# Kernel optimization log

Measured on AMD Instinct MI355X. Metric: run time of the kernel, lower is better.

Reference implementation:

```python
import jax, jax.numpy as jnp
import numpy as np

B, T, DM, DF, E, K = 4, 1024, 768, 3072, 8, 2


def setup_inputs() -> dict:
    key = jax.random.key(0)
    k0, k1, k2, k3 = jax.random.split(key, 4)
    x = jax.random.normal(k0, (B, T, DM), jnp.float32)
    Wg = jax.random.normal(k1, (DM, E), jnp.float32) * 0.02
    W1 = jax.random.normal(k2, (E, DM, DF), jnp.float32) * 0.02
    b1 = jnp.zeros((E, DF), jnp.float32)
    W2 = jax.random.normal(k3, (E, DF, DM), jnp.float32) * 0.02
    b2 = jnp.zeros((E, DM), jnp.float32)
    return {"x": x, "Wg": Wg, "W1": W1, "b1": b1, "W2": W2, "b2": b2}


def reference(x, Wg, W1, b1, W2, b2):
    # --- flatten (s)equence x (t)oken -> S tokens of width m ---
    m = x.shape[-1]
    xs = x.reshape(-1, m)              # [S, m]
    S = xs.shape[0]
    n_exp = W1.shape[0]

    # --- top-k softmax gate: combine_weights [k,S], dispatch order sorted by expert ---
    logits = xs @ Wg                   # [S, E]
    probs = jax.nn.softmax(logits, axis=-1)
    topv, topi = jax.lax.top_k(probs, K)                 # [S, K]
    cw = topv / jnp.sum(topv, axis=-1, keepdims=True)    # renormalize top-k
    combine_weights = cw.T                               # [K, S]

    # slot layout: slot = j*S + s (matches rerouted_output.reshape(k, S, m))
    eid_flat = topi.T.reshape(-1)                        # [S*K] expert id per slot
    dispatch_mask = jnp.argsort(eid_flat)                # stable sort by expert == chunked order
    e_sorted = eid_flat[dispatch_mask]                   # [S*K] sorted expert ids

    # --- dispatch: gather token rows (dispatch_mask % S indexes the token) ---
    dispatched = xs[dispatch_mask % S]                   # [S*K, m]

    # --- experts: per-expert FFN; loop over fixed small expert count, masked combine ---
    expert_outputs = jnp.zeros_like(dispatched)
    for e in range(n_exp):
        sel = (e_sorted == e)[:, None].astype(dispatched.dtype)
        h = jax.nn.relu(dispatched @ W1[e] + b1[e])      # [S*K, DF]
        expert_outputs = expert_outputs + sel * (h @ W2[e] + b2[e])

    # --- scatter back to slot order, then weighted combine over k ---
    rerouted = jnp.zeros((S * K, m), expert_outputs.dtype).at[dispatch_mask].set(expert_outputs)
    rerouted = rerouted.reshape(K, S, m)
    combined = jnp.einsum('ks,ksm->sm', combine_weights, rerouted)
    return combined.reshape(x.shape).astype(x.dtype)
```

## Files before the change

### kernel.cpp

```cpp
#include <hip/hip_runtime.h>
#include <math.h>

typedef short short8 __attribute__((ext_vector_type(8)));
typedef float f32x4 __attribute__((ext_vector_type(4)));
typedef unsigned short u16;
typedef unsigned int u32;

#define S_TOK 4096
#define DM 768
#define DF 3072
#define NE 8
#define NSLOT (S_TOK*2)
#define PSLOT 9216
#define MBMAX 72

#define WS_COUNTS   0
#define WS_CURSOR   512
#define WS_OFFS     1024
#define WS_MBE      1088
#define WS_EID      2048
#define WS_GW       (WS_EID + NSLOT*4)
#define WS_POS      (WS_GW  + NSLOT*4)
#define WS_TOK      (WS_POS + NSLOT*4)
#define CTRL_BYTES  262144

#define AS1 __attribute__((address_space(1)))
#define AS3 __attribute__((address_space(3)))
#define GLDS16(g, s) __builtin_amdgcn_global_load_lds((const AS1 u32*)(g), (AS3 u32*)(s), 16, 0, 0)

__device__ inline u16 f2b(float f){
    u32 u = __builtin_bit_cast(u32, f);
    u32 r = (u + 0x7fffu + ((u >> 16) & 1u)) >> 16;
    return (u16)r;
}

__global__ __launch_bounds__(256) void cvtw_kernel(const float* __restrict__ W1, u16* __restrict__ W1s,
                                                   const float* __restrict__ W2, u16* __restrict__ W2s,
                                                   int* __restrict__ counts, int* __restrict__ cursor){
    if (blockIdx.x == 0 && blockIdx.y == 0 && threadIdx.x < 128){
        counts[threadIdx.x] = 0; cursor[threadIdx.x] = 0;
    }
    int e = blockIdx.y;
    int b = blockIdx.x;
    const float* Wp; u16* Wsp; int Kd, Nd;
    if (b < 576){ Wp = W1; Wsp = W1s; Kd = DM; Nd = DF; }
    else        { b -= 576; Wp = W2; Wsp = W2s; Kd = DF; Nd = DM; }
    int kbn = Kd >> 5;
    Wp  += (size_t)e*Kd*Nd;
    Wsp += (size_t)e*Kd*Nd;
    int t = threadIdx.x;
    int u = b*256 + t;
    int l   = u & 63;
    int kb  = (u >> 6) % kbn;
    int qq  = (u >> 6) / kbn;
    int ntp = qq & 3;
    int nb  = qq >> 2;
    int k0 = kb*32 + (l >> 4)*8;
    int c  = nb*128 + ntp*32 + (l & 15);
    const float* src = Wp + (size_t)k0*Nd + c;
    short8 o0, o1;
#pragma unroll
    for (int j = 0; j < 8; j++){
        o0[j] = (short)f2b(src[(size_t)j*Nd]);
        o1[j] = (short)f2b(src[(size_t)j*Nd + 16]);
    }
    size_t v0 = ((size_t)(nb*8 + ntp*2)*kbn + kb)*64 + l;
    *(short8*)&Wsp[v0*8] = o0;
    *(short8*)&Wsp[v0*8 + (size_t)kbn*512] = o1;
}

#define GATE_BLOCKS 128
__global__ __launch_bounds__(256) void gate_kernel(const float* __restrict__ x, const float* __restrict__ Wg,
                                                   int* __restrict__ eid, float* __restrict__ gw,
                                                   int* __restrict__ counts, u16* __restrict__ xb){
    __shared__ int lh[NE];
    int t = threadIdx.x;
    if (t < NE) lh[t] = 0;
    __syncthreads();
    int wv = t >> 6, l = t & 63;
    int wgid = blockIdx.x*4 + wv;
    const int NW = GATE_BLOCKS*4;

    for (int s = wgid; s < S_TOK; s += NW){
        float acc[NE];
#pragma unroll
        for (int e = 0; e < NE; e++) acc[e] = 0.f;
        const float* xr = x + (size_t)s * DM;
        u16* xbr = xb + (size_t)s * DM;
#pragma unroll
        for (int i = 0; i < DM/64; i++){
            int d = l + 64*i;
            float xv = xr[d];
            xbr[d] = f2b(xv);
            float4 w0 = *(const float4*)(Wg + d*NE);
            float4 w1 = *(const float4*)(Wg + d*NE + 4);
            acc[0] += xv*w0.x; acc[1] += xv*w0.y; acc[2] += xv*w0.z; acc[3] += xv*w0.w;
            acc[4] += xv*w1.x; acc[5] += xv*w1.y; acc[6] += xv*w1.z; acc[7] += xv*w1.w;
        }
#pragma unroll
        for (int e = 0; e < NE; e++){
#pragma unroll
            for (int off = 32; off; off >>= 1) acc[e] += __shfl_down(acc[e], off);
        }
        if (l == 0){
            int i1 = 0; float v1 = acc[0];
            for (int e = 1; e < NE; e++) if (acc[e] > v1){ v1 = acc[e]; i1 = e; }
            int i2 = -1; float v2 = -1e30f;
            for (int e = 0; e < NE; e++) if (e != i1 && acc[e] > v2){ v2 = acc[e]; i2 = e; }
            float w0, w1;
            if (i2 < 0){ i2 = (i1 + 1) & 7; w0 = 1.f; w1 = 0.f; }
            else {
                float e2 = expf(v2 - v1);
                w0 = 1.f / (1.f + e2);
                w1 = e2 / (1.f + e2);
            }
            eid[2*s]   = i1; gw[2*s]   = w0;
            eid[2*s+1] = i2; gw[2*s+1] = w1;
            atomicAdd(&lh[i1], 1);
            atomicAdd(&lh[i2], 1);
        }
    }
    __syncthreads();
    if (t < NE && lh[t] > 0) atomicAdd(&counts[t*16], lh[t]);
}

__global__ void offsets_kernel(const int* __restrict__ counts, int* __restrict__ offs,
                               int* __restrict__ cursor, int* __restrict__ mbe){
    if (threadIdx.x == 0 && blockIdx.x == 0){
        int P = 0;
        for (int e = 0; e < NE; e++){
            offs[e] = P; cursor[e*16] = P;
            int padded = ((counts[e*16] + 127) >> 7) << 7;
            for (int mb = P >> 7; mb < (P + padded) >> 7; mb++) mbe[mb] = e;
            P += padded;
        }
        offs[NE] = P;
        for (int mb = P >> 7; mb < MBMAX; mb++) mbe[mb] = -1;
    }
}

__global__ __launch_bounds__(256) void scatter_kernel(const int* __restrict__ eid, int* __restrict__ cursor,
                                                      const int* __restrict__ counts, const int* __restrict__ offs,
                                                      const int* __restrict__ mbe,
                                                      int* __restrict__ tok_of, int* __restrict__ pos_of){
    __shared__ int lh[NE];
    __shared__ int base[NE];
    int t = threadIdx.x;
    if (t < NE) lh[t] = 0;
    __syncthreads();
    int i = blockIdx.x*256 + t;
    int e = 0, r = 0;
    if (i < NSLOT){
        e = eid[i];
        if (e < 0) e = 0; if (e > 7) e = 7;
        r = atomicAdd(&lh[e], 1);
    }
    __syncthreads();
    if (t < NE) base[t] = (lh[t] > 0) ? atomicAdd(&cursor[t*16], lh[t]) : 0;
    __syncthreads();
    if (i < NSLOT){
        int p = base[e] + r;
        if (p < 0) p = 0; if (p >= PSLOT) p = PSLOT - 1;
        tok_of[p] = i >> 1;
        pos_of[i] = p;
    }
    int p = i;
    int pe = mbe[p >> 7];
    if (pe < 0){ tok_of[p] = 0; }
    else if (p >= offs[pe] + counts[pe*16]){ tok_of[p] = 0; }
}

__global__ __launch_bounds__(256) void gemm1p_kernel(const u16* __restrict__ xb, const int* __restrict__ tok_of,
                                                     const int* __restrict__ mbe, const u16* __restrict__ W1s,
                                                     const float* __restrict__ b1, u16* __restrict__ h){
    const int KB = DM/32;
    const int NT = DM/64;
    int bid = blockIdx.x;
    int by = bid % 24, mb = bid / 24;
    int e = mbe[mb];
    if (e < 0) return;
    int m0 = mb*128, n0 = by*128;

    int t = threadIdx.x;
    int w = t >> 6, l = t & 63;
    int wm = w & 1, wn = w >> 1;

    __shared__ u16 As[128*72];
    __shared__ u16 Bs[2*2*8*512];

    int row0 = t >> 2, kc = t & 3;
    const u16* a0 = xb + (size_t)tok_of[m0 + row0]*DM + kc*8;
    const u16* a1 = xb + (size_t)tok_of[m0 + row0 + 64]*DM + kc*8;
    u16* as0 = &As[row0*72 + kc*8];
    u16* as1 = &As[(row0 + 64)*72 + kc*8];

    const u16* bbase = W1s + (size_t)e*DM*DF + (size_t)(((n0 >> 4) + 2*w)*KB)*512 + l*8;

#define STB1(kb2, buf) do{ \
    GLDS16(bbase + (size_t)(2*(kb2))*512,                   &Bs[(buf)*8192 + (2*w)*512]); \
    GLDS16(bbase + (size_t)(2*(kb2)+1)*512,                 &Bs[(buf)*8192 + 4096 + (2*w)*512]); \
    GLDS16(bbase + (size_t)KB*512 + (size_t)(2*(kb2))*512,  &Bs[(buf)*8192 + (2*w+1)*512]); \
    GLDS16(bbase + (size_t)KB*512 + (size_t)(2*(kb2)+1)*512,&Bs[(buf)*8192 + 4096 + (2*w+1)*512]); \
}while(0)

    f32x4 acc[4][4];
#pragma unroll
    for (int i = 0; i < 4; i++)
#pragma unroll
        for (int j = 0; j < 4; j++) acc[i][j] = (f32x4){0.f,0.f,0.f,0.f};

    short8 av0a = *(const short8*)a0;
    short8 av0b = *(const short8*)(a0 + 32);
    short8 av1a = *(const short8*)a1;
    short8 av1b = *(const short8*)(a1 + 32);
    STB1(0, 0);
    *(short8*)as0 = av0a; *(short8*)(as0 + 32) = av0b;
    *(short8*)as1 = av1a; *(short8*)(as1 + 32) = av1b;
    av0a = *(const short8*)(a0 + 64);
    av0b = *(const short8*)(a0 + 96);
    av1a = *(const short8*)(a1 + 64);
    av1b = *(const short8*)(a1 + 96);
    __builtin_amdgcn_sched_barrier(0);
    asm volatile("s_waitcnt vmcnt(4) lgkmcnt(0)" ::: "memory");
    __builtin_amdgcn_sched_barrier(0);
    __builtin_amdgcn_s_barrier();

    int cb = 0;
    for (int kt = 0; kt < NT; kt++){
        if (kt + 1 < NT) STB1(kt + 1, cb ^ 1);
#pragma unroll
        for (int ks = 0; ks < 2; ks++){
            short8 af[4], bf[4];
#pragma unroll
            for (int mt = 0; mt < 4; mt++)
                af[mt] = *(const short8*)&As[(wm*64 + mt*16 + (l & 15))*72 + ks*32 + (l >> 4)*8];
#pragma unroll
            for (int nt = 0; nt < 4; nt++)
                bf[nt] = *(const short8*)&Bs[cb*8192 + ks*4096 + (wn*4 + nt)*512 + l*8];
#pragma unroll
            for (int mt = 0; mt < 4; mt++)
#pragma unroll
                for (int nt = 0; nt < 4; nt++)
                    acc[mt][nt] = __builtin_amdgcn_mfma_f32_16x16x32_bf16(af[mt], bf[nt], acc[mt][nt], 0, 0, 0);
        }
        __builtin_amdgcn_sched_barrier(0);
        asm volatile("s_waitcnt vmcnt(4) lgkmcnt(0)" ::: "memory");
        __builtin_amdgcn_sched_barrier(0);
        __builtin_amdgcn_s_barrier();
        if (kt + 1 < NT){
            *(short8*)as0 = av0a; *(short8*)(as0 + 32) = av0b;
            *(short8*)as1 = av1a; *(short8*)(as1 + 32) = av1b;
            if (kt + 2 < NT){
                av0a = *(const short8*)(a0 + (kt+2)*64);
                av0b = *(const short8*)(a0 + (kt+2)*64 + 32);
                av1a = *(const short8*)(a1 + (kt+2)*64);
                av1b = *(const short8*)(a1 + (kt+2)*64 + 32);
                __builtin_amdgcn_sched_barrier(0);
                asm volatile("s_waitcnt vmcnt(4) lgkmcnt(0)" ::: "memory");
                __builtin_amdgcn_sched_barrier(0);
            } else {
                __builtin_amdgcn_sched_barrier(0);
                asm volatile("s_waitcnt vmcnt(0) lgkmcnt(0)" ::: "memory");
                __builtin_amdgcn_sched_barrier(0);
            }
            __builtin_amdgcn_s_barrier();
        }
        cb ^= 1;
    }
#undef STB1

#pragma unroll
    for (int nt = 0; nt < 4; nt++){
        int col = n0 + wn*64 + nt*16 + (l & 15);
        float bv = b1[e*DF + col];
#pragma unroll
        for (int mt = 0; mt < 4; mt++){
#pragma unroll
            for (int r = 0; r < 4; r++){
                int grow = m0 + wm*64 + mt*16 + (l >> 4)*4 + r;
                float v = acc[mt][nt][r] + bv;
                v = v > 0.f ? v : 0.f;
                h[(size_t)grow*DF + col] = f2b(v);
            }
        }
    }
}

__global__ __launch_bounds__(256) void gemm2p_kernel(const u16* __restrict__ h, const int* __restrict__ mbe,
                                                     const u16* __restrict__ W2s, const float* __restrict__ b2,
                                                     float* __restrict__ y){
    const int KB = DF/32;
    const int NT = DF/64;
    int bid = blockIdx.x;
    int mb = bid % MBMAX;
    int by = bid / MBMAX;
    int e = mbe[mb];
    if (e < 0) return;
    int m0 = mb*128, n0 = by*128;

    int t = threadIdx.x;
    int w = t >> 6, l = t & 63;
    int wm = w & 1, wn = w >> 1;

    __shared__ u16 As[128*72];
    __shared__ u16 Bs[3*2*8*512];

    int row0 = t >> 2, kc = t & 3;
    const u16* a0 = h + (size_t)(m0 + row0)*DF + kc*8;
    const u16* a1 = h + (size_t)(m0 + row0 + 64)*DF + kc*8;
    u16* as0 = &As[row0*72 + kc*8];
    u16* as1 = &As[(row0 + 64)*72 + kc*8];

    const u16* bbase = W2s + (size_t)e*DF*DM + (size_t)(((n0 >> 4) + 2*w)*KB)*512 + l*8;

#define STB2(kb2, buf) do{ \
    GLDS16(bbase + (size_t)(2*(kb2))*512,                   &Bs[(buf)*8192 + (2*w)*512]); \
    GLDS16(bbase + (size_t)(2*(kb2)+1)*512,                 &Bs[(buf)*8192 + 4096 + (2*w)*512]); \
    GLDS16(bbase + (size_t)KB*512 + (size_t)(2*(kb2))*512,  &Bs[(buf)*8192 + (2*w+1)*512]); \
    GLDS16(bbase + (size_t)KB*512 + (size_t)(2*(kb2)+1)*512,&Bs[(buf)*8192 + 4096 + (2*w+1)*512]); \
}while(0)

    f32x4 acc[4][4];
#pragma unroll
    for (int i = 0; i < 4; i++)
#pragma unroll
        for (int j = 0; j < 4; j++) acc[i][j] = (f32x4){0.f,0.f,0.f,0.f};

    short8 av0a = *(const short8*)a0;
    short8 av0b = *(const short8*)(a0 + 32);
    short8 av1a = *(const short8*)a1;
    short8 av1b = *(const short8*)(a1 + 32);
    STB2(0, 0);
    STB2(1, 1);
    *(short8*)as0 = av0a; *(short8*)(as0 + 32) = av0b;
    *(short8*)as1 = av1a; *(short8*)(as1 + 32) = av1b;
    av0a = *(const short8*)(a0 + 64);
    av0b = *(const short8*)(a0 + 96);
    av1a = *(const short8*)(a1 + 64);
    av1b = *(const short8*)(a1 + 96);
    __builtin_amdgcn_sched_barrier(0);
    asm volatile("s_waitcnt vmcnt(8) lgkmcnt(0)" ::: "memory");
    __builtin_amdgcn_sched_barrier(0);
    __builtin_amdgcn_s_barrier();

    int cb = 0, sb = 2;
    for (int kt = 0; kt < NT; kt++){
        if (kt + 2 < NT) STB2(kt + 2, sb);
#pragma unroll
        for (int ks = 0; ks < 2; ks++){
            short8 af[4], bf[4];
#pragma unroll
            for (int mt = 0; mt < 4; mt++)
                af[mt] = *(const short8*)&As[(wm*64 + mt*16 + (l & 15))*72 + ks*32 + (l >> 4)*8];
#pragma unroll
            for (int nt = 0; nt < 4; nt++)
                bf[nt] = *(const short8*)&Bs[cb*8192 + ks*4096 + (wn*4 + nt)*512 + l*8];
#pragma unroll
            for (int mt = 0; mt < 4; mt++)
#pragma unroll
                for (int nt = 0; nt < 4; nt++)
                    acc[mt][nt] = __builtin_amdgcn_mfma_f32_16x16x32_bf16(af[mt], bf[nt], acc[mt][nt], 0, 0, 0);
        }
        __builtin_amdgcn_sched_barrier(0);
        asm volatile("s_waitcnt vmcnt(4) lgkmcnt(0)" ::: "memory");
        __builtin_amdgcn_sched_barrier(0);
        __builtin_amdgcn_s_barrier();
        if (kt + 1 < NT){
            *(short8*)as0 = av0a; *(short8*)(as0 + 32) = av0b;
            *(short8*)as1 = av1a; *(short8*)(as1 + 32) = av1b;
            if (kt + 2 < NT){
                av0a = *(const short8*)(a0 + (kt+2)*64);
                av0b = *(const short8*)(a0 + (kt+2)*64 + 32);
                av1a = *(const short8*)(a1 + (kt+2)*64);
                av1b = *(const short8*)(a1 + (kt+2)*64 + 32);
            }
            __builtin_amdgcn_sched_barrier(0);
            asm volatile("s_waitcnt lgkmcnt(0)" ::: "memory");
            __builtin_amdgcn_sched_barrier(0);
            __builtin_amdgcn_s_barrier();
        }
        cb = (cb == 2) ? 0 : cb + 1;
        sb = (sb == 2) ? 0 : sb + 1;
    }
#undef STB2

#pragma unroll
    for (int nt = 0; nt < 4; nt++){
        int col = n0 + wn*64 + nt*16 + (l & 15);
        float bv = b2[e*DM + col];
#pragma unroll
        for (int mt = 0; mt < 4; mt++){
#pragma unroll
            for (int r = 0; r < 4; r++){
                int grow = m0 + wm*64 + mt*16 + (l >> 4)*4 + r;
                y[(size_t)grow*DM + col] = acc[mt][nt][r] + bv;
            }
        }
    }
}

__global__ __launch_bounds__(256) void combine_kernel(const float* __restrict__ y, const int* __restrict__ pos_of,
                                                      const float* __restrict__ gw, float* __restrict__ out){
    int i = blockIdx.x*256 + threadIdx.x;
    int s = i / (DM/4);
    int c4 = (i - s*(DM/4))*4;
    int p0 = pos_of[2*s], p1 = pos_of[2*s+1];
    float w0 = gw[2*s], w1 = gw[2*s+1];
    float4 a = *(const float4*)&y[(size_t)p0*DM + c4];
    float4 b = *(const float4*)&y[(size_t)p1*DM + c4];
    float4 o;
    o.x = w0*a.x + w1*b.x;
    o.y = w0*a.y + w1*b.y;
    o.z = w0*a.z + w1*b.z;
    o.w = w0*a.w + w1*b.w;
    *(float4*)&out[(size_t)s*DM + c4] = o;
}

__global__ __launch_bounds__(256) void fallback_kernel(const float* __restrict__ x, const float* __restrict__ Wg,
                                                       const float* __restrict__ W1, const float* __restrict__ b1,
                                                       const float* __restrict__ W2, const float* __restrict__ b2,
                                                       float* __restrict__ out){
    int s = blockIdx.x;
    int t = threadIdx.x;
    __shared__ float xr[DM];
    __shared__ float hl[DF];
    __shared__ float yl[DM];
    __shared__ float lacc[4*NE];
    __shared__ int   sel_e[2];
    __shared__ float sel_w[2];

    for (int i = t; i < DM; i += 256){ xr[i] = x[(size_t)s*DM + i]; yl[i] = 0.f; }
    __syncthreads();

    float acc[NE];
#pragma unroll
    for (int e = 0; e < NE; e++) acc[e] = 0.f;
    for (int d = t*3; d < t*3 + 3; d++){
        float xv = xr[d];
#pragma unroll
        for (int e = 0; e < NE; e++) acc[e] += xv * Wg[d*NE + e];
    }
#pragma unroll
    for (int e = 0; e < NE; e++){
#pragma unroll
        for (int off = 32; off; off >>= 1) acc[e] += __shfl_down(acc[e], off);
    }
    if ((t & 63) == 0){
        int wv = t >> 6;
#pragma unroll
        for (int e = 0; e < NE; e++) lacc[wv*NE + e] = acc[e];
    }
    __syncthreads();
    if (t == 0){
        float lg[NE];
#pragma unroll
        for (int e = 0; e < NE; e++) lg[e] = lacc[e] + lacc[NE + e] + lacc[2*NE + e] + lacc[3*NE + e];
        int i1 = 0; float v1 = lg[0];
        for (int e = 1; e < NE; e++) if (lg[e] > v1){ v1 = lg[e]; i1 = e; }
        int i2 = -1; float v2 = -1e30f;
        for (int e = 0; e < NE; e++) if (e != i1 && lg[e] > v2){ v2 = lg[e]; i2 = e; }
        if (i2 < 0){ i2 = (i1 + 1) & 7; sel_w[0] = 1.f; sel_w[1] = 0.f; }
        else {
            float e2 = expf(v2 - v1);
            sel_w[0] = 1.f / (1.f + e2);
            sel_w[1] = e2 / (1.f + e2);
        }
        sel_e[0] = i1; sel_e[1] = i2;
    }
    __syncthreads();

    for (int kk = 0; kk < 2; kk++){
        int e = sel_e[kk];
        float wgt = sel_w[kk];
        const float* w1p = W1 + (size_t)e * DM * DF;
        for (int j = t; j < DF; j += 256){
            float a = b1[e*DF + j];
            for (int k = 0; k < DM; k++) a += xr[k] * w1p[(size_t)k*DF + j];
            hl[j] = a > 0.f ? a : 0.f;
        }
        __syncthreads();
        const float* w2p = W2 + (size_t)e * DF * DM;
        for (int c = t; c < DM; c += 256){
            float a = b2[e*DM + c];
            for (int k = 0; k < DF; k++) a += hl[k] * w2p[(size_t)k*DM + c];
            yl[c] += wgt * a;
        }
        __syncthreads();
    }
    for (int c = t; c < DM; c += 256) out[(size_t)s*DM + c] = yl[c];
}

extern "C" void kernel_launch(void* const* d_in, const int* in_sizes, int n_in,
                              void* d_out, int out_size, void* d_ws, size_t ws_size,
                              hipStream_t stream) {
    const float* x  = (const float*)d_in[0];
    const float* Wg = (const float*)d_in[1];
    const float* W1 = (const float*)d_in[2];
    const float* b1 = (const float*)d_in[3];
    const float* W2 = (const float*)d_in[4];
    const float* b2 = (const float*)d_in[5];
    float* out = (float*)d_out;

    char* ws = (char*)d_ws;
    int*   counts = (int*)(ws + WS_COUNTS);
    int*   cursor = (int*)(ws + WS_CURSOR);
    int*   offs   = (int*)(ws + WS_OFFS);
    int*   mbe    = (int*)(ws + WS_MBE);
    int*   eid    = (int*)(ws + WS_EID);
    float* gw     = (float*)(ws + WS_GW);
    int*   pos_of = (int*)(ws + WS_POS);
    int*   tok_of = (int*)(ws + WS_TOK);

    const size_t xbB = (size_t)S_TOK*DM*2;
    const size_t wB  = (size_t)NE*DM*DF*2;
    const size_t hB  = (size_t)PSLOT*DF*2;
    const size_t need = CTRL_BYTES + xbB + 2*wB + hB;

    if (ws_size < need){
        fallback_kernel<<<S_TOK, 256, 0, stream>>>(x, Wg, W1, b1, W2, b2, out);
        return;
    }

    u16* xb  = (u16*)(ws + CTRL_BYTES);
    u16* W1s = (u16*)(ws + CTRL_BYTES + xbB);
    u16* W2s = (u16*)(ws + CTRL_BYTES + xbB + wB);
    u16* h   = (u16*)(ws + CTRL_BYTES + xbB + 2*wB);
    float* yb = (float*)(ws + CTRL_BYTES + xbB);

    cvtw_kernel<<<dim3(1152, NE), 256, 0, stream>>>(W1, W1s, W2, W2s, counts, cursor);
    gate_kernel<<<GATE_BLOCKS, 256, 0, stream>>>(x, Wg, eid, gw, counts, xb);
    offsets_kernel<<<1, 1, 0, stream>>>(counts, offs, cursor, mbe);
    scatter_kernel<<<PSLOT/256, 256, 0, stream>>>(eid, cursor, counts, offs, mbe, tok_of, pos_of);

    gemm1p_kernel<<<MBMAX*24, 256, 0, stream>>>(xb, tok_of, mbe, W1s, b1, h);
    gemm2p_kernel<<<6*MBMAX, 256, 0, stream>>>(h, mbe, W2s, b2, yb);
    combine_kernel<<<(S_TOK*(DM/4))/256, 256, 0, stream>>>(yb, pos_of, gw, out);
}
```

Baseline: 344.4 us.

## Drop offsets kernel and double-buffer A tiles to cut GEMM barriers

Removes the single-thread offsets kernel. Expert offsets and the row-block-to-expert mapping are now recomputed inline from counts in the scatter and GEMM kernels, with the cursor used as a relative offset. Both grouped GEMMs now double-buffer the A tile in LDS and stage the next A and B tiles before the MFMA loop, so each k-step needs one barrier instead of two. gemm2 drops its three-deep B ring for a two-deep one, which gives up some prefetch depth on the long K loop.

Result: slower. 355.4 us (+3.2%).

```diff
diff --git a/kernel.cpp b/kernel.cpp
--- a/kernel.cpp
+++ b/kernel.cpp
@@ -16,8 +16,6 @@
 
 #define WS_COUNTS   0
 #define WS_CURSOR   512
-#define WS_OFFS     1024
-#define WS_MBE      1088
 #define WS_EID      2048
 #define WS_GW       (WS_EID + NSLOT*4)
 #define WS_POS      (WS_GW  + NSLOT*4)
@@ -32,6 +30,17 @@
     u32 u = __builtin_bit_cast(u32, f);
     u32 r = (u + 0x7fffu + ((u >> 16) & 1u)) >> 16;
     return (u16)r;
+}
+
+__device__ inline int expert_of_row(const int* __restrict__ counts, int m0base){
+    int e = -1, P = 0;
+#pragma unroll
+    for (int q = 0; q < NE; q++){
+        int padded = ((counts[q*16] + 127) >> 7) << 7;
+        if (m0base >= P && m0base < P + padded) e = q;
+        P += padded;
+    }
+    return e;
 }
 
 __global__ __launch_bounds__(256) void cvtw_kernel(const float* __restrict__ W1, u16* __restrict__ W1s,
@@ -124,29 +133,19 @@
     if (t < NE && lh[t] > 0) atomicAdd(&counts[t*16], lh[t]);
 }
 
-__global__ void offsets_kernel(const int* __restrict__ counts, int* __restrict__ offs,
-                               int* __restrict__ cursor, int* __restrict__ mbe){
-    if (threadIdx.x == 0 && blockIdx.x == 0){
-        int P = 0;
-        for (int e = 0; e < NE; e++){
-            offs[e] = P; cursor[e*16] = P;
-            int padded = ((counts[e*16] + 127) >> 7) << 7;
-            for (int mb = P >> 7; mb < (P + padded) >> 7; mb++) mbe[mb] = e;
-            P += padded;
-        }
-        offs[NE] = P;
-        for (int mb = P >> 7; mb < MBMAX; mb++) mbe[mb] = -1;
-    }
-}
-
 __global__ __launch_bounds__(256) void scatter_kernel(const int* __restrict__ eid, int* __restrict__ cursor,
-                                                      const int* __restrict__ counts, const int* __restrict__ offs,
-                                                      const int* __restrict__ mbe,
+                                                      const int* __restrict__ counts,
                                                       int* __restrict__ tok_of, int* __restrict__ pos_of){
     __shared__ int lh[NE];
     __shared__ int base[NE];
+    __shared__ int offsP[NE+1];
     int t = threadIdx.x;
     if (t < NE) lh[t] = 0;
+    if (t == 0){
+        int P = 0;
+        for (int q = 0; q < NE; q++){ offsP[q] = P; P += ((counts[q*16] + 127) >> 7) << 7; }
+        offsP[NE] = P;
+    }
     __syncthreads();
     int i = blockIdx.x*256 + t;
     int e = 0, r = 0;
@@ -156,7 +155,7 @@
         r = atomicAdd(&lh[e], 1);
     }
     __syncthreads();
-    if (t < NE) base[t] = (lh[t] > 0) ? atomicAdd(&cursor[t*16], lh[t]) : 0;
+    if (t < NE) base[t] = offsP[t] + ((lh[t] > 0) ? atomicAdd(&cursor[t*16], lh[t]) : 0);
     __syncthreads();
     if (i < NSLOT){
         int p = base[e] + r;
@@ -164,20 +163,22 @@
         tok_of[p] = i >> 1;
         pos_of[i] = p;
     }
-    int p = i;
-    int pe = mbe[p >> 7];
-    if (pe < 0){ tok_of[p] = 0; }
-    else if (p >= offs[pe] + counts[pe*16]){ tok_of[p] = 0; }
+    int p2 = i;
+    int pe = -1;
+#pragma unroll
+    for (int q = 0; q < NE; q++) if (p2 >= offsP[q] && p2 < offsP[q+1]) pe = q;
+    if (pe < 0){ tok_of[p2] = 0; }
+    else if (p2 >= offsP[pe] + counts[pe*16]){ tok_of[p2] = 0; }
 }
 
 __global__ __launch_bounds__(256) void gemm1p_kernel(const u16* __restrict__ xb, const int* __restrict__ tok_of,
-                                                     const int* __restrict__ mbe, const u16* __restrict__ W1s,
+                                                     const int* __restrict__ counts, const u16* __restrict__ W1s,
                                                      const float* __restrict__ b1, u16* __restrict__ h){
     const int KB = DM/32;
     const int NT = DM/64;
     int bid = blockIdx.x;
     int by = bid % 24, mb = bid / 24;
-    int e = mbe[mb];
+    int e = expert_of_row(counts, mb*128);
     if (e < 0) return;
     int m0 = mb*128, n0 = by*128;
 
@@ -185,14 +186,14 @@
     int w = t >> 6, l = t & 63;
     int wm = w & 1, wn = w >> 1;
 
-    __shared__ u16 As[128*72];
+    __shared__ u16 As[2*128*72];
     __shared__ u16 Bs[2*2*8*512];
 
     int row0 = t >> 2, kc = t & 3;
     const u16* a0 = xb + (size_t)tok_of[m0 + row0]*DM + kc*8;
     const u16* a1 = xb + (size_t)tok_of[m0 + row0 + 64]*DM + kc*8;
-    u16* as0 = &As[row0*72 + kc*8];
-    u16* as1 = &As[(row0 + 64)*72 + kc*8];
+    int aso0 = row0*72 + kc*8;
+    int aso1 = (row0 + 64)*72 + kc*8;
 
     const u16* bbase = W1s + (size_t)e*DM*DF + (size_t)(((n0 >> 4) + 2*w)*KB)*512 + l*8;
 
@@ -213,9 +214,9 @@
     short8 av0b = *(const short8*)(a0 + 32);
     short8 av1a = *(const short8*)a1;
     short8 av1b = *(const short8*)(a1 + 32);
+    *(short8*)&As[aso0] = av0a; *(short8*)&As[aso0 + 32] = av0b;
+    *(short8*)&As[aso1] = av1a; *(short8*)&As[aso1 + 32] = av1b;
     STB1(0, 0);
-    *(short8*)as0 = av0a; *(short8*)(as0 + 32) = av0b;
-    *(short8*)as1 = av1a; *(short8*)(as1 + 32) = av1b;
     av0a = *(const short8*)(a0 + 64);
     av0b = *(const short8*)(a0 + 96);
     av1a = *(const short8*)(a1 + 64);
@@ -225,47 +226,42 @@
     __builtin_amdgcn_sched_barrier(0);
     __builtin_amdgcn_s_barrier();
 
-    int cb = 0;
     for (int kt = 0; kt < NT; kt++){
-        if (kt + 1 < NT) STB1(kt + 1, cb ^ 1);
-#pragma unroll
-        for (int ks = 0; ks < 2; ks++){
-            short8 af[4], bf[4];
-#pragma unroll
-            for (int mt = 0; mt < 4; mt++)
-                af[mt] = *(const short8*)&As[(wm*64 + mt*16 + (l & 15))*72 + ks*32 + (l >> 4)*8];
-#pragma unroll
-            for (int nt = 0; nt < 4; nt++)
-                bf[nt] = *(const short8*)&Bs[cb*8192 + ks*4096 + (wn*4 + nt)*512 + l*8];
-#pragma unroll
-            for (int mt = 0; mt < 4; mt++)
-#pragma unroll
-                for (int nt = 0; nt < 4; nt++)
-                    acc[mt][nt] = __builtin_amdgcn_mfma_f32_16x16x32_bf16(af[mt], bf[nt], acc[mt][nt], 0, 0, 0);
-        }
-        __builtin_amdgcn_sched_barrier(0);
-        asm volatile("s_waitcnt vmcnt(4) lgkmcnt(0)" ::: "memory");
-        __builtin_amdgcn_sched_barrier(0);
-        __builtin_amdgcn_s_barrier();
+        int p = kt & 1, q = p ^ 1;
         if (kt + 1 < NT){
-            *(short8*)as0 = av0a; *(short8*)(as0 + 32) = av0b;
-            *(short8*)as1 = av1a; *(short8*)(as1 + 32) = av1b;
+            *(short8*)&As[q*9216 + aso0] = av0a; *(short8*)&As[q*9216 + aso0 + 32] = av0b;
+            *(short8*)&As[q*9216 + aso1] = av1a; *(short8*)&As[q*9216 + aso1 + 32] = av1b;
+            STB1(kt + 1, q);
             if (kt + 2 < NT){
                 av0a = *(const short8*)(a0 + (kt+2)*64);
                 av0b = *(const short8*)(a0 + (kt+2)*64 + 32);
                 av1a = *(const short8*)(a1 + (kt+2)*64);
                 av1b = *(const short8*)(a1 + (kt+2)*64 + 32);
-                __builtin_amdgcn_sched_barrier(0);
-                asm volatile("s_waitcnt vmcnt(4) lgkmcnt(0)" ::: "memory");
-                __builtin_amdgcn_sched_barrier(0);
-            } else {
-                __builtin_amdgcn_sched_barrier(0);
-                asm volatile("s_waitcnt vmcnt(0) lgkmcnt(0)" ::: "memory");
-                __builtin_amdgcn_sched_barrier(0);
             }
-            __builtin_amdgcn_s_barrier();
-        }
-        cb ^= 1;
+        }
+#pragma unroll
+        for (int ks = 0; ks < 2; ks++){
+            short8 af[4], bf[4];
+#pragma unroll
+            for (int mt = 0; mt < 4; mt++)
+                af[mt] = *(const short8*)&As[p*9216 + (wm*64 + mt*16 + (l & 15))*72 + ks*32 + (l >> 4)*8];
+#pragma unroll
+            for (int nt = 0; nt < 4; nt++)
+                bf[nt] = *(const short8*)&Bs[p*8192 + ks*4096 + (wn*4 + nt)*512 + l*8];
+#pragma unroll
+            for (int mt = 0; mt < 4; mt++)
+#pragma unroll
+                for (int nt = 0; nt < 4; nt++)
+                    acc[mt][nt] = __builtin_amdgcn_mfma_f32_16x16x32_bf16(af[mt], bf[nt], acc[mt][nt], 0, 0, 0);
+        }
+        __builtin_amdgcn_sched_barrier(0);
+        if (kt + 2 < NT){
+            asm volatile("s_waitcnt vmcnt(4) lgkmcnt(0)" ::: "memory");
+        } else {
+            asm volatile("s_waitcnt vmcnt(0) lgkmcnt(0)" ::: "memory");
+        }
+        __builtin_amdgcn_sched_barrier(0);
+        __builtin_amdgcn_s_barrier();
     }
 #undef STB1
 
@@ -286,7 +282,7 @@
     }
 }
 
-__global__ __launch_bounds__(256) void gemm2p_kernel(const u16* __restrict__ h, const int* __restrict__ mbe,
+__global__ __launch_bounds__(256) void gemm2p_kernel(const u16* __restrict__ h, const int* __restrict__ counts,
                                                      const u16* __restrict__ W2s, const float* __restrict__ b2,
                                                      float* __restrict__ y){
     const int KB = DF/32;
@@ -294,7 +290,7 @@
     int bid = blockIdx.x;
     int mb = bid % MBMAX;
     int by = bid / MBMAX;
-    int e = mbe[mb];
+    int e = expert_of_row(counts, mb*128);
     if (e < 0) return;
     int m0 = mb*128, n0 = by*128;
 
@@ -302,14 +298,14 @@
     int w = t >> 6, l = t & 63;
     int wm = w & 1, wn = w >> 1;
 
-    __shared__ u16 As[128*72];
-    __shared__ u16 Bs[3*2*8*512];
+    __shared__ u16 As[2*128*72];
+    __shared__ u16 Bs[2*2*8*512];
 
     int row0 = t >> 2, kc = t & 3;
     const u16* a0 = h + (size_t)(m0 + row0)*DF + kc*8;
     const u16* a1 = h + (size_t)(m0 + row0 + 64)*DF + kc*8;
-    u16* as0 = &As[row0*72 + kc*8];
-    u16* as1 = &As[(row0 + 64)*72 + kc*8];
+    int aso0 = row0*72 + kc*8;
+    int aso1 = (row0 + 64)*72 + kc*8;
 
     const u16* bbase = W2s + (size_t)e*DF*DM + (size_t)(((n0 >> 4) + 2*w)*KB)*512 + l*8;
 
@@ -330,57 +326,54 @@
     short8 av0b = *(const short8*)(a0 + 32);
     short8 av1a = *(const short8*)a1;
     short8 av1b = *(const short8*)(a1 + 32);
+    *(short8*)&As[aso0] = av0a; *(short8*)&As[aso0 + 32] = av0b;
+    *(short8*)&As[aso1] = av1a; *(short8*)&As[aso1 + 32] = av1b;
     STB2(0, 0);
-    STB2(1, 1);
-    *(short8*)as0 = av0a; *(short8*)(as0 + 32) = av0b;
-    *(short8*)as1 = av1a; *(short8*)(as1 + 32) = av1b;
     av0a = *(const short8*)(a0 + 64);
     av0b = *(const short8*)(a0 + 96);
     av1a = *(const short8*)(a1 + 64);
     av1b = *(const short8*)(a1 + 96);
     __builtin_amdgcn_sched_barrier(0);
-    asm volatile("s_waitcnt vmcnt(8) lgkmcnt(0)" ::: "memory");
+    asm volatile("s_waitcnt vmcnt(4) lgkmcnt(0)" ::: "memory");
     __builtin_amdgcn_sched_barrier(0);
     __builtin_amdgcn_s_barrier();
 
-    int cb = 0, sb = 2;
     for (int kt = 0; kt < NT; kt++){
-        if (kt + 2 < NT) STB2(kt + 2, sb);
-#pragma unroll
-        for (int ks = 0; ks < 2; ks++){
-            short8 af[4], bf[4];
-#pragma unroll
-            for (int mt = 0; mt < 4; mt++)
-                af[mt] = *(const short8*)&As[(wm*64 + mt*16 + (l & 15))*72 + ks*32 + (l >> 4)*8];
-#pragma unroll
-            for (int nt = 0; nt < 4; nt++)
-                bf[nt] = *(const short8*)&Bs[cb*8192 + ks*4096 + (wn*4 + nt)*512 + l*8];
-#pragma unroll
-            for (int mt = 0; mt < 4; mt++)
-#pragma unroll
-                for (int nt = 0; nt < 4; nt++)
-                    acc[mt][nt] = __builtin_amdgcn_mfma_f32_16x16x32_bf16(af[mt], bf[nt], acc[mt][nt], 0, 0, 0);
-        }
-        __builtin_amdgcn_sched_barrier(0);
-        asm volatile("s_waitcnt vmcnt(4) lgkmcnt(0)" ::: "memory");
-        __builtin_amdgcn_sched_barrier(0);
-        __builtin_amdgcn_s_barrier();
+        int p = kt & 1, q = p ^ 1;
         if (kt + 1 < NT){
-            *(short8*)as0 = av0a; *(short8*)(as0 + 32) = av0b;
-            *(short8*)as1 = av1a; *(short8*)(as1 + 32) = av1b;
+            *(short8*)&As[q*9216 + aso0] = av0a; *(short8*)&As[q*9216 + aso0 + 32] = av0b;
+            *(short8*)&As[q*9216 + aso1] = av1a; *(short8*)&As[q*9216 + aso1 + 32] = av1b;
+            STB2(kt + 1, q);
             if (kt + 2 < NT){
                 av0a = *(const short8*)(a0 + (kt+2)*64);
                 av0b = *(const short8*)(a0 + (kt+2)*64 + 32);
                 av1a = *(const short8*)(a1 + (kt+2)*64);
                 av1b = *(const short8*)(a1 + (kt+2)*64 + 32);
             }
-            __builtin_amdgcn_sched_barrier(0);
-            asm volatile("s_waitcnt lgkmcnt(0)" ::: "memory");
-            __builtin_amdgcn_sched_barrier(0);
-            __builtin_amdgcn_s_barrier();
-        }
-        cb = (cb == 2) ? 0 : cb + 1;
-        sb = (sb == 2) ? 0 : sb + 1;
+        }
+#pragma unroll
+        for (int ks = 0; ks < 2; ks++){
+            short8 af[4], bf[4];
+#pragma unroll
+            for (int mt = 0; mt < 4; mt++)
+                af[mt] = *(const short8*)&As[p*9216 + (wm*64 + mt*16 + (l & 15))*72 + ks*32 + (l >> 4)*8];
+#pragma unroll
+            for (int nt = 0; nt < 4; nt++)
+                bf[nt] = *(const short8*)&Bs[p*8192 + ks*4096 + (wn*4 + nt)*512 + l*8];
+#pragma unroll
+            for (int mt = 0; mt < 4; mt++)
+#pragma unroll
+                for (int nt = 0; nt < 4; nt++)
+                    acc[mt][nt] = __builtin_amdgcn_mfma_f32_16x16x32_bf16(af[mt], bf[nt], acc[mt][nt], 0, 0, 0);
+        }
+        __builtin_amdgcn_sched_barrier(0);
+        if (kt + 2 < NT){
+            asm volatile("s_waitcnt vmcnt(4) lgkmcnt(0)" ::: "memory");
+        } else {
+            asm volatile("s_waitcnt vmcnt(0) lgkmcnt(0)" ::: "memory");
+        }
+        __builtin_amdgcn_sched_barrier(0);
+        __builtin_amdgcn_s_barrier();
     }
 #undef STB2
 
@@ -504,8 +497,6 @@
     char* ws = (char*)d_ws;
     int*   counts = (int*)(ws + WS_COUNTS);
     int*   cursor = (int*)(ws + WS_CURSOR);
-    int*   offs   = (int*)(ws + WS_OFFS);
-    int*   mbe    = (int*)(ws + WS_MBE);
     int*   eid    = (int*)(ws + WS_EID);
     float* gw     = (float*)(ws + WS_GW);
     int*   pos_of = (int*)(ws + WS_POS);
@@ -529,10 +520,9 @@
 
     cvtw_kernel<<<dim3(1152, NE), 256, 0, stream>>>(W1, W1s, W2, W2s, counts, cursor);
     gate_kernel<<<GATE_BLOCKS, 256, 0, stream>>>(x, Wg, eid, gw, counts, xb);
-    offsets_kernel<<<1, 1, 0, stream>>>(counts, offs, cursor, mbe);
-    scatter_kernel<<<PSLOT/256, 256, 0, stream>>>(eid, cursor, counts, offs, mbe, tok_of, pos_of);
-
-    gemm1p_kernel<<<MBMAX*24, 256, 0, stream>>>(xb, tok_of, mbe, W1s, b1, h);
-    gemm2p_kernel<<<6*MBMAX, 256, 0, stream>>>(h, mbe, W2s, b2, yb);
+    scatter_kernel<<<PSLOT/256, 256, 0, stream>>>(eid, cursor, counts, tok_of, pos_of);
+
+    gemm1p_kernel<<<MBMAX*24, 256, 0, stream>>>(xb, tok_of, counts, W1s, b1, h);
+    gemm2p_kernel<<<6*MBMAX, 256, 0, stream>>>(h, counts, W2s, b2, yb);
     combine_kernel<<<(S_TOK*(DM/4))/256, 256, 0, stream>>>(yb, pos_of, gw, out);
 }
```
